# Performance work log

Measured on AMD Instinct MI355X. Metric: run time of the kernel, lower is better.

The kernel has to match this reference:

```python
import jax, jax.numpy as jnp
import numpy as np

B, T, A, H, E = 256, 64, 32, 512, 32


def setup_inputs() -> dict:
    key = jax.random.key(0)
    ks = jax.random.split(key, 8)
    return {
        "actions": jax.random.normal(ks[0], (B, T, A), dtype=jnp.float32),
        "timesteps": jax.random.randint(ks[1], (B,), 0, 1000, dtype=jnp.int32),
        "cat_ids": jax.random.randint(ks[2], (B,), 0, E, dtype=jnp.int32),
        "W1": 0.02 * jax.random.normal(ks[3], (E, A, H), dtype=jnp.float32),
        "b1": jnp.zeros((E, H), dtype=jnp.float32),
        "W2": 0.02 * jax.random.normal(ks[4], (E, 2 * H, H), dtype=jnp.float32),
        "b2": jnp.zeros((E, H), dtype=jnp.float32),
        "W3": 0.02 * jax.random.normal(ks[5], (E, H, H), dtype=jnp.float32),
        "b3": jnp.zeros((E, H), dtype=jnp.float32),
    }


def _cat_linear(x, cat_ids, W, b):
    # per-sample weight gather + bmm, faithful to torch W[cat_ids]; bmm
    return jnp.einsum("btd,bdh->bth", x, W[cat_ids]) + b[cat_ids][:, None, :]


def _sinusoidal(timesteps_bt, dim):
    half = dim // 2
    exponent = -jnp.arange(half, dtype=jnp.float32) * (jnp.log(jnp.float32(10000.0)) / half)
    freqs = timesteps_bt[..., None] * jnp.exp(exponent)  # (B,T,half)
    return jnp.concatenate([jnp.sin(freqs), jnp.cos(freqs)], axis=-1)


def _swish(x):
    return x * jax.nn.sigmoid(x)


def reference(actions, timesteps, cat_ids, W1, b1, W2, b2, W3, b3):
    Bb, Tt, _ = actions.shape
    t_bt = jnp.broadcast_to(timesteps.astype(jnp.float32)[:, None], (Bb, Tt))
    a_emb = _cat_linear(actions, cat_ids, W1, b1)                     # (B,T,H)
    tau_emb = _sinusoidal(t_bt, a_emb.shape[-1]).astype(a_emb.dtype)  # (B,T,H)
    x = jnp.concatenate([a_emb, tau_emb], axis=-1)                    # (B,T,2H)
    x = _swish(_cat_linear(x, cat_ids, W2, b2))
    return _cat_linear(x, cat_ids, W3, b3)
```

## Files before the change

kernel.cpp:

```cpp
#include <hip/hip_runtime.h>
#include <hip/hip_bf16.h>

#define NB 256
#define NT 64
#define NA 32
#define NH 512
#define NE 32
#define MAXTILES 144

typedef short short8 __attribute__((ext_vector_type(8)));
typedef unsigned short ushort8v __attribute__((ext_vector_type(8)));
typedef float f32x4 __attribute__((ext_vector_type(4)));

__device__ __forceinline__ unsigned short f2bf(float f) {
  unsigned int u = __float_as_uint(f);
  u += 0x7FFFu + ((u >> 16) & 1u);
  return (unsigned short)(u >> 16);
}

__device__ __forceinline__ void gl2lds16(const void* g, void* l) {
  __builtin_amdgcn_global_load_lds(
      (const __attribute__((address_space(1))) unsigned int*)g,
      (__attribute__((address_space(3))) unsigned int*)l, 16, 0, 0);
}

__device__ __forceinline__ ushort8v cvt8(float4 a, float4 b) {
  ushort8v t;
  t[0] = f2bf(a.x); t[1] = f2bf(a.y); t[2] = f2bf(a.z); t[3] = f2bf(a.w);
  t[4] = f2bf(b.x); t[5] = f2bf(b.y); t[6] = f2bf(b.z); t[7] = f2bf(b.w);
  return t;
}

__device__ __forceinline__ void pf_w2(float2 (&pf)[8], const float* __restrict__ W2en,
                                      int k0, int tid) {
#pragma unroll
  for (int j = 0; j < 8; j++) {
    int u = j * 256 + tid;
    int kk = u >> 5, cc = u & 31;
    pf[j] = *(const float2*)(W2en + ((size_t)(k0 + kk) << 9) + cc * 2);
  }
}

__device__ __forceinline__ void pf_w1(float4 (&pfw)[2], const float* __restrict__ W1e,
                                      int k0, int tid) {
  int a = tid >> 3, p = tid & 7;
  const float* src = W1e + (size_t)a * NH + k0 + p * 8;
  pfw[0] = *(const float4*)src;
  pfw[1] = *(const float4*)(src + 4);
}

__global__ __launch_bounds__(256) void wp_kernel(
    const float* __restrict__ W1, const float* __restrict__ b1,
    const float* __restrict__ W2, const float* __restrict__ b2,
    const float* __restrict__ W3, const int* __restrict__ timesteps,
    const int* __restrict__ cat, unsigned short* __restrict__ Wt12,
    float* __restrict__ bias2G, float* __restrict__ tvec,
    unsigned short* __restrict__ Wt3, int* __restrict__ tiles,
    int* __restrict__ ntiles_out) {
  __shared__ __align__(16) unsigned char smem[43008];
  int tid = threadIdx.x;
  int bx = blockIdx.x;

  if (bx >= 512 && bx < 2560) {
    float* S = (float*)smem;
    int id = bx - 512;
    int e = id >> 6, rem = id & 63;
    int nt = (rem & 7) * 64, kt = (rem >> 3) * 64;
#pragma unroll
    for (int j = 0; j < 8; j++) {
      int u = j * 256 + tid;
      int k = u >> 5, c = u & 31;
      float2 v = *(const float2*)(W3 + ((size_t)e * 512 + kt + k) * NH + nt + 2 * c);
      *(float2*)(&S[k * 66 + 2 * c]) = v;
    }
    __syncthreads();
#pragma unroll
    for (int j = 0; j < 2; j++) {
      int u = j * 256 + tid;
      int n = u >> 3, c = u & 7;
      ushort8v pk;
#pragma unroll
      for (int jj = 0; jj < 8; jj++) pk[jj] = f2bf(S[(c * 8 + jj) * 66 + n]);
      *(ushort8v*)(Wt3 + ((size_t)e * NH + nt + n) * 512 + kt + c * 8) = pk;
    }
    return;
  }

  if (bx == 2560) {
    int* cnt = (int*)smem;
    int* off = cnt + 32;
    int* cur = off + 32;
    int* order = cur + 32;
    if (tid < NE) cnt[tid] = 0;
    __syncthreads();
    int e = cat[tid];
    atomicAdd(&cnt[e], 1);
    __syncthreads();
    if (tid == 0) {
      int s = 0;
      for (int i = 0; i < NE; i++) { off[i] = s; cur[i] = s; s += cnt[i]; }
    }
    __syncthreads();
    int p = atomicAdd(&cur[e], 1);
    order[p] = tid;
    __syncthreads();
    if (tid == 0) {
      int nt = 0;
      for (int i = 0; i < NE; i++) {
        for (int j = 0; j < cnt[i]; j += 2) {
          tiles[3 * nt + 0] = i;
          tiles[3 * nt + 1] = order[off[i] + j];
          tiles[3 * nt + 2] = (j + 1 < cnt[i]) ? order[off[i] + j + 1] : -1;
          nt++;
        }
      }
      *ntiles_out = nt;
    }
    return;
  }

  int w = tid >> 6, l = tid & 63;
  int lrow = l & 15, kq = l >> 4;
  int tn = tid & 63, tp = tid >> 6;

  if (bx < 256) {
    float* S            = (float*)smem;
    unsigned short* Bs  = (unsigned short*)(smem + 16896);
    unsigned short* As  = (unsigned short*)(smem + 25088);
    float* b1S          = (float*)(smem + 29184);
    float* bias2P       = (float*)(smem + 31232);

    int e = bx >> 3, n0 = (bx & 7) * 64;
    const float* W2en = W2 + ((size_t)e << 19) + n0;
    const float* W1e = W1 + ((size_t)e << 14);

    {
      float2 v = *(const float2*)(b1 + (size_t)e * NH + tid * 2);
      *(float2*)(&b1S[tid * 2]) = v;
    }

    float2 pf[2][8];
    float4 pfW[2][2];
    pf_w2(pf[0], W2en, 0, tid);
    pf_w1(pfW[0], W1e, 0, tid);

    f32x4 acc1[2];
    acc1[0] = (f32x4){0.f, 0.f, 0.f, 0.f};
    acc1[1] = (f32x4){0.f, 0.f, 0.f, 0.f};
    float bacc0 = 0.f, bacc1 = 0.f;

#pragma unroll
    for (int chunk = 0; chunk < 8; chunk++) {
      const int cur = chunk & 1, nxt = cur ^ 1;
      __syncthreads();
#pragma unroll
      for (int j = 0; j < 8; j++) {
        int u = j * 256 + tid;
        int kk = u >> 5, cc = u & 31;
        *(float2*)(&S[kk * 66 + cc * 2]) = pf[cur][j];
      }
      {
        int a = tid >> 3, p = tid & 7;
        *(ushort8v*)(&As[a * 64 + (p ^ (a & 7)) * 8]) = cvt8(pfW[cur][0], pfW[cur][1]);
      }
      if (chunk < 7) {
        pf_w2(pf[nxt], W2en, (chunk + 1) * 64, tid);
        pf_w1(pfW[nxt], W1e, (chunk + 1) * 64, tid);
      }
      __syncthreads();
#pragma unroll
      for (int i2 = 0; i2 < 2; i2++) {
        int p = tp + i2 * 4;
        ushort8v pk;
        float bsum = 0.f;
#pragma unroll
        for (int jj = 0; jj < 8; jj++) {
          float sv = S[(p * 8 + jj) * 66 + tn];
          pk[jj] = f2bf(sv);
          bsum += sv * b1S[chunk * 64 + p * 8 + jj];
        }
        *(ushort8v*)(&Bs[tn * 64 + (p ^ (tn & 7)) * 8]) = pk;
        if (i2 == 0) bacc0 += bsum; else bacc1 += bsum;
      }
      __syncthreads();
#pragma unroll
      for (int s2 = 0; s2 < 2; s2++) {
        int nrow = w * 16 + lrow;
        short8 bf = *(short8*)(&Bs[nrow * 64 + (((s2 * 4 + kq) ^ (nrow & 7))) * 8]);
#pragma unroll
        for (int mi = 0; mi < 2; mi++) {
          int ar = mi * 16 + lrow;
          short8 af = *(short8*)(&As[ar * 64 + (((s2 * 4 + kq) ^ (ar & 7))) * 8]);
          acc1[mi] = __builtin_amdgcn_mfma_f32_16x16x32_bf16(af, bf, acc1[mi], 0, 0, 0);
        }
      }
    }

    unsigned short* Sb = (unsigned short*)S;
#pragma unroll
    for (int mi = 0; mi < 2; mi++)
#pragma unroll
      for (int r = 0; r < 4; r++)
        Sb[(w * 16 + lrow) * 40 + mi * 16 + kq * 4 + r] = f2bf(acc1[mi][r]);
    bias2P[tn * 8 + tp] = bacc0;
    bias2P[tn * 8 + tp + 4] = bacc1;
    __syncthreads();
    if (tid < 64) {
      float s = b2[(size_t)e * NH + n0 + tid];
#pragma unroll
      for (int p2 = 0; p2 < 8; p2++) s += bias2P[tid * 8 + p2];
      bias2G[(size_t)e * NH + n0 + tid] = s;
    }
    {
      int n = tid >> 2, q = tid & 3;
      ushort8v v = *(ushort8v*)(&Sb[n * 40 + q * 8]);
      *(ushort8v*)(Wt12 + ((size_t)(e * NH) + n0 + n) * NA + q * 8) = v;
    }
    return;
  }

  {
    float* S            = (float*)smem;
    unsigned short* Bs  = (unsigned short*)(smem + 16896);
    unsigned short* tauS= (unsigned short*)(smem + 25088);
    int* list           = (int*)(smem + 41728);
    int* pcnt           = (int*)(smem + 42752);

    int id = bx - 256;
    int e = id >> 3, n0 = (id & 7) * 64;
    const float* W2bn = W2 + ((size_t)e << 19) + ((size_t)512 << 9) + n0;

    if (tid == 0) *pcnt = 0;
    __syncthreads();
    {
      int ce = cat[tid];
      if (ce == e) { int p = atomicAdd(pcnt, 1); list[p] = tid; }
    }
    __syncthreads();
    int c = *pcnt;
    if (c == 0) return;

    const float kLog = 0.035977893400931146f;
    float2 pf[2][8];

    for (int sg = 0; sg * 16 < c; sg++) {
      if (sg > 0) __syncthreads();
      for (int j = 0; j < 32; j++) {
        int u = j * 256 + tid;
        int s = u >> 9, k = u & 511;
        int si = sg * 16 + s;
        float t = (si < c) ? (float)timesteps[list[si]] : 0.f;
        float f = expf(-(float)(k & 255) * kLog);
        float ang = t * f;
        tauS[s * 520 + k] = f2bf((k < 256) ? sinf(ang) : cosf(ang));
      }
      pf_w2(pf[0], W2bn, 0, tid);
      f32x4 acc2 = (f32x4){0.f, 0.f, 0.f, 0.f};
#pragma unroll
      for (int chunk = 0; chunk < 8; chunk++) {
        const int cur = chunk & 1, nxt = cur ^ 1;
        __syncthreads();
#pragma unroll
        for (int j = 0; j < 8; j++) {
          int u = j * 256 + tid;
          int kk = u >> 5, cc = u & 31;
          *(float2*)(&S[kk * 66 + cc * 2]) = pf[cur][j];
        }
        if (chunk < 7) pf_w2(pf[nxt], W2bn, (chunk + 1) * 64, tid);
        __syncthreads();
#pragma unroll
        for (int i2 = 0; i2 < 2; i2++) {
          int p = tp + i2 * 4;
          ushort8v pk;
#pragma unroll
          for (int jj = 0; jj < 8; jj++) pk[jj] = f2bf(S[(p * 8 + jj) * 66 + tn]);
          *(ushort8v*)(&Bs[tn * 64 + (p ^ (tn & 7)) * 8]) = pk;
        }
        __syncthreads();
#pragma unroll
        for (int s2 = 0; s2 < 2; s2++) {
          int nrow = w * 16 + lrow;
          short8 bf = *(short8*)(&Bs[nrow * 64 + (((s2 * 4 + kq) ^ (nrow & 7))) * 8]);
          short8 af = *(short8*)(&tauS[lrow * 520 + chunk * 64 + s2 * 32 + kq * 8]);
          acc2 = __builtin_amdgcn_mfma_f32_16x16x32_bf16(af, bf, acc2, 0, 0, 0);
        }
      }
#pragma unroll
      for (int r = 0; r < 4; r++) {
        int si = sg * 16 + kq * 4 + r;
        if (si < c)
          tvec[(size_t)list[si] * NH + n0 + w * 16 + lrow] = acc2[r];
      }
    }
  }
}

__global__ __launch_bounds__(256) void gemmh_kernel(
    const float* __restrict__ actions, const unsigned short* __restrict__ Wt12,
    const float* __restrict__ tvec, const float* __restrict__ bias2,
    const int* __restrict__ cat_ids, unsigned short* __restrict__ Hb) {
  __shared__ __align__(16) unsigned char smem[16384 + 5120 + 33792];
  unsigned short* Ws = (unsigned short*)smem;
  unsigned short* As = (unsigned short*)(smem + 16384);
  unsigned short* Ts = (unsigned short*)(smem + 16384 + 5120);

  int b = blockIdx.y, h = blockIdx.x;
  int tid = threadIdx.x;
  int e = cat_ids[b];

  {
    const unsigned short* wsrc = Wt12 + ((size_t)e * NH + h * 256) * NA;
#pragma unroll
    for (int j = 0; j < 4; j++) {
      int u = j * 256 + tid;
      int n = u >> 2, p = u & 3;
      int ch = p ^ ((n >> 1) & 3);
      gl2lds16(wsrc + (size_t)n * NA + ch * 8,
               Ws + (size_t)(j * 256 + (tid & 448)) * 8);
    }
  }
  {
    int row = tid >> 2, seg = tid & 3;
    const float* src = actions + (size_t)(b * NT + row) * NA + seg * 8;
    float4 v0 = *(const float4*)(src);
    float4 v1 = *(const float4*)(src + 4);
    *(ushort8v*)(&As[row * 40 + seg * 8]) = cvt8(v0, v1);
  }
  __syncthreads();

  int w = tid >> 6, l = tid & 63;
  int lrow = l & 15, kq = l >> 4;
  short8 af = *(short8*)(&As[(w * 16 + lrow) * 40 + kq * 8]);
  f32x4 zero = {0.f, 0.f, 0.f, 0.f};
  f32x4 acc[16];
#pragma unroll
  for (int ni = 0; ni < 16; ni++) {
    int nn = ni * 16 + lrow;
    int p = kq ^ ((nn >> 1) & 3);
    short8 bfv = *(short8*)(&Ws[nn * 32 + p * 8]);
    acc[ni] = __builtin_amdgcn_mfma_f32_16x16x32_bf16(af, bfv, zero, 0, 0, 0);
  }
#pragma unroll
  for (int ni = 0; ni < 16; ni++) {
    int colL = ni * 16 + lrow;
    float bv = tvec[(size_t)b * NH + h * 256 + colL] +
               bias2[(size_t)e * NH + h * 256 + colL];
#pragma unroll
    for (int r = 0; r < 4; r++) {
      int row = w * 16 + kq * 4 + r;
      float v = acc[ni][r] + bv;
      v = v / (1.0f + __expf(-v));
      Ts[row * 264 + colL] = f2bf(v);
    }
  }
  __syncthreads();
#pragma unroll
  for (int i = 0; i < 8; i++) {
    int u = i * 256 + tid;
    int t = u >> 5, c4 = u & 31;
    uint4 v = *(uint4*)(&Ts[t * 264 + c4 * 8]);
    *(uint4*)(Hb + ((size_t)(b * NT + t)) * NH + h * 256 + c4 * 8) = v;
  }
}

template <int KTOT, bool HASTAU, bool SWISH, bool OUT_BF16>
__global__ __launch_bounds__(256) void gemm2_kernel(
    const unsigned short* __restrict__ Xa, const unsigned short* __restrict__ Xt,
    const unsigned short* __restrict__ Wt, const float* __restrict__ bias,
    void* __restrict__ Yv, const int* __restrict__ tiles,
    const int* __restrict__ pntiles) {
  __shared__ __align__(16) unsigned char smem[49152];

  int ti = blockIdx.y;
  if (ti >= *pntiles) return;
  int n0 = blockIdx.x * 64;
  int e = tiles[3 * ti], s0 = tiles[3 * ti + 1], s1 = tiles[3 * ti + 2];
  int s1v = (s1 < 0) ? s0 : s1;

  int tid = threadIdx.x;
  int l = tid & 63;
  int wr = (tid >> 7), wc = (tid >> 6) & 1;
  int lrow = l & 15, kq = l >> 4;

  const unsigned short* wbase = Wt + ((size_t)e * NH + n0) * KTOT;
  constexpr int NIT = KTOT / 64;

  auto stage = [&](int it, int buf) {
    unsigned short* As = (unsigned short*)(smem + buf * 24576);
    unsigned short* Bs = (unsigned short*)(smem + buf * 24576 + 16384);
    int k0 = it * 64;
#pragma unroll
    for (int j = 0; j < 4; j++) {
      int u = j * 256 + tid;
      int row = u >> 3, p = u & 7;
      int ch = p ^ (row & 7);
      int kk = k0 + ch * 8;
      int s = (row < 64) ? s0 : s1v;
      const unsigned short* src;
      if (HASTAU && kk >= 512)
        src = Xt + (size_t)s * NH + (kk - 512);
      else
        src = Xa + ((size_t)(s * NT + (row & 63))) * NH + kk;
      gl2lds16(src, As + (size_t)(j * 256 + (tid & 448)) * 8);
    }
#pragma unroll
    for (int j = 0; j < 2; j++) {
      int u = j * 256 + tid;
      int n = u >> 3, p = u & 7;
      int ch = p ^ (n & 7);
      gl2lds16(wbase + (size_t)n * KTOT + k0 + ch * 8,
               Bs + (size_t)(j * 256 + (tid & 448)) * 8);
    }
  };

  f32x4 acc[4][2];
#pragma unroll
  for (int mi = 0; mi < 4; mi++)
#pragma unroll
    for (int ni = 0; ni < 2; ni++) acc[mi][ni] = (f32x4){0.f, 0.f, 0.f, 0.f};

  stage(0, 0);
  stage(1, 1);

  for (int t = 0; t < NIT; t++) {
    int cur = t & 1;
    unsigned short* As = (unsigned short*)(smem + cur * 24576);
    unsigned short* Bs = (unsigned short*)(smem + cur * 24576 + 16384);

    if (t + 1 < NIT) {
      asm volatile("s_waitcnt vmcnt(6)" ::: "memory");
    } else {
      asm volatile("s_waitcnt vmcnt(0)" ::: "memory");
    }
    __builtin_amdgcn_sched_barrier(0);
    __builtin_amdgcn_s_barrier();
    __builtin_amdgcn_sched_barrier(0);

    short8 afr[2][4], bfr[2][2];
#pragma unroll
    for (int s2 = 0; s2 < 2; s2++) {
#pragma unroll
      for (int mi = 0; mi < 4; mi++) {
        int row = wr * 64 + mi * 16 + lrow;
        int p = (s2 * 4 + kq) ^ (row & 7);
        afr[s2][mi] = *(short8*)(&As[row * 64 + p * 8]);
      }
#pragma unroll
      for (int ni = 0; ni < 2; ni++) {
        int n = wc * 32 + ni * 16 + lrow;
        int p = (s2 * 4 + kq) ^ (n & 7);
        bfr[s2][ni] = *(short8*)(&Bs[n * 64 + p * 8]);
      }
    }
    asm volatile("s_waitcnt lgkmcnt(0)" ::: "memory");
    __builtin_amdgcn_sched_barrier(0);
    __builtin_amdgcn_s_barrier();
    __builtin_amdgcn_sched_barrier(0);

    if (t + 2 < NIT) stage(t + 2, cur);

#pragma unroll
    for (int s2 = 0; s2 < 2; s2++)
#pragma unroll
      for (int mi = 0; mi < 4; mi++)
#pragma unroll
        for (int ni = 0; ni < 2; ni++)
          acc[mi][ni] = __builtin_amdgcn_mfma_f32_16x16x32_bf16(
              afr[s2][mi], bfr[s2][ni], acc[mi][ni], 0, 0, 0);
  }
  __syncthreads();

#pragma unroll
  for (int ni = 0; ni < 2; ni++) {
    int colL = wc * 32 + ni * 16 + lrow;
    float bv = bias[(size_t)e * NH + n0 + colL];
#pragma unroll
    for (int mi = 0; mi < 4; mi++) {
#pragma unroll
      for (int r = 0; r < 4; r++) {
        int row = wr * 64 + mi * 16 + kq * 4 + r;
        float v = acc[mi][ni][r] + bv;
        if (SWISH) v = v / (1.0f + __expf(-v));
        if (OUT_BF16)
          ((unsigned short*)smem)[row * 80 + colL] = f2bf(v);
        else
          ((float*)smem)[row * 68 + colL] = v;
      }
    }
  }
  __syncthreads();
  if (OUT_BF16) {
    unsigned short* Y = (unsigned short*)Yv;
#pragma unroll
    for (int i = 0; i < 4; i++) {
      int u = i * 256 + tid;
      int row = u >> 3, c = u & 7;
      if (row >= 64 && s1 < 0) continue;
      int s = (row < 64) ? s0 : s1;
      uint4 v = *(uint4*)(&((unsigned short*)smem)[row * 80 + c * 8]);
      *(uint4*)(Y + ((size_t)(s * NT + (row & 63))) * NH + n0 + c * 8) = v;
    }
  } else {
    float* Y = (float*)Yv;
#pragma unroll
    for (int i = 0; i < 8; i++) {
      int u = i * 256 + tid;
      int row = u >> 4, c = u & 15;
      if (row >= 64 && s1 < 0) continue;
      int s = (row < 64) ? s0 : s1;
      uint4 v = *(uint4*)(&((float*)smem)[row * 68 + c * 4]);
      *(uint4*)(Y + ((size_t)(s * NT + (row & 63))) * NH + n0 + c * 4) = v;
    }
  }
}

extern "C" void kernel_launch(void* const* d_in, const int* in_sizes, int n_in,
                              void* d_out, int out_size, void* d_ws, size_t ws_size,
                              hipStream_t stream) {
  const float* actions   = (const float*)d_in[0];
  const int*   timesteps = (const int*)d_in[1];
  const int*   cat_ids   = (const int*)d_in[2];
  const float* W1 = (const float*)d_in[3];
  const float* b1 = (const float*)d_in[4];
  const float* W2 = (const float*)d_in[5];
  const float* b2 = (const float*)d_in[6];
  const float* W3 = (const float*)d_in[7];
  const float* b3 = (const float*)d_in[8];

  unsigned short* Hb   = (unsigned short*)d_ws;
  unsigned short* Wt3  = (unsigned short*)((char*)d_ws + (size_t)16777216);
  unsigned short* Wt12 = (unsigned short*)((char*)d_ws + (size_t)33554432);
  float* tvec  = (float*)((char*)d_ws + (size_t)34603008);
  float* bias2 = (float*)((char*)d_ws + (size_t)35127296);
  int* tiles   = (int*)((char*)d_ws + (size_t)35192832);
  int* ntiles  = tiles + 3 * MAXTILES;

  wp_kernel<<<2561, 256, 0, stream>>>(W1, b1, W2, b2, W3, timesteps, cat_ids,
                                      Wt12, bias2, tvec, Wt3, tiles, ntiles);
  gemmh_kernel<<<dim3(2, NB), 256, 0, stream>>>(actions, Wt12, tvec, bias2,
                                                cat_ids, Hb);
  gemm2_kernel<512, false, false, false><<<dim3(8, MAXTILES), 256, 0, stream>>>(
      Hb, nullptr, Wt3, b3, d_out, tiles, ntiles);
}
```

Before: 195.4 us.

## Widen weight-prep blocks to 256 columns and re-tile W3 as k-blocked layout

The weight-prep kernel changes from 64-column tiles over many small blocks to 256-column tiles with a shared streaming helper that pipelines W2 reads two chunks ahead. The W1·W2 fold and tau projection now process 32 rows per pass. The W3 transpose writes a k-blocked [e][kb][n][64] layout, and gemm2 indexes that layout. The goal is fewer blocks, less redundant W1/tau work and more MFMA work per W2 load, at the cost of fewer blocks in flight (641 vs 2561) and more LDS per block.

```diff
diff --git a/kernel.cpp b/kernel.cpp
--- a/kernel.cpp
+++ b/kernel.cpp
@@ -31,25 +31,78 @@
   return t;
 }
 
-__device__ __forceinline__ void pf_w2(float2 (&pf)[8], const float* __restrict__ W2en,
-                                      int k0, int tid) {
+__device__ __forceinline__ void pfld(float2 (&pf)[8], const float* __restrict__ base,
+                                     int c, int tid) {
 #pragma unroll
   for (int j = 0; j < 8; j++) {
     int u = j * 256 + tid;
-    int kk = u >> 5, cc = u & 31;
-    pf[j] = *(const float2*)(W2en + ((size_t)(k0 + kk) << 9) + cc * 2);
-  }
-}
-
-__device__ __forceinline__ void pf_w1(float4 (&pfw)[2], const float* __restrict__ W1e,
-                                      int k0, int tid) {
-  int a = tid >> 3, p = tid & 7;
-  const float* src = W1e + (size_t)a * NH + k0 + p * 8;
-  pfw[0] = *(const float4*)src;
-  pfw[1] = *(const float4*)(src + 4);
-}
-
-__global__ __launch_bounds__(256) void wp_kernel(
+    int kk = u >> 7, cc = u & 127;
+    pf[j] = *(const float2*)(base + (size_t)(c * 16 + kk) * NH + cc * 2);
+  }
+}
+
+template <bool BIASDOT>
+__device__ __forceinline__ void stream_block(
+    const float* __restrict__ Wbase, float* S, unsigned short* Bs,
+    const unsigned short* As, const float* b1S, int tid, int w, int lrow,
+    int kq, f32x4 (&acc)[2][4], float& bacc) {
+  float2 pf[2][8];
+  pfld(pf[0], Wbase, 0, tid);
+  pfld(pf[1], Wbase, 1, tid);
+#pragma unroll 2
+  for (int c = 0; c < 32; c++) {
+    const int cur = c & 1;
+    __syncthreads();
+#pragma unroll
+    for (int j = 0; j < 8; j++) {
+      int u = j * 256 + tid;
+      int kk = u >> 7, cc = u & 127;
+      *(float2*)(&S[kk * 260 + cc * 2]) = pf[cur][j];
+    }
+    if (c + 2 < 32) pfld(pf[cur], Wbase, c + 2, tid);
+    __syncthreads();
+    {
+      int n = tid;
+      ushort8v pk0, pk1;
+#pragma unroll
+      for (int kk = 0; kk < 8; kk++) {
+        float sv = S[kk * 260 + n];
+        pk0[kk] = f2bf(sv);
+        if (BIASDOT) bacc += sv * b1S[c * 16 + kk];
+      }
+#pragma unroll
+      for (int kk = 8; kk < 16; kk++) {
+        float sv = S[kk * 260 + n];
+        pk1[kk - 8] = f2bf(sv);
+        if (BIASDOT) bacc += sv * b1S[c * 16 + kk];
+      }
+      *(ushort8v*)(&Bs[n * 40 + cur * 16]) = pk0;
+      *(ushort8v*)(&Bs[n * 40 + cur * 16 + 8]) = pk1;
+    }
+    if (cur) {
+      __syncthreads();
+      int w2i = c >> 1;
+      short8 bf[4], af[2];
+#pragma unroll
+      for (int ni = 0; ni < 4; ni++)
+        bf[ni] = *(short8*)(&Bs[(w * 64 + ni * 16 + lrow) * 40 + kq * 8]);
+#pragma unroll
+      for (int mi = 0; mi < 2; mi++) {
+        int a = mi * 16 + lrow;
+        int ck = w2i * 4 + kq;
+        af[mi] = *(short8*)(&As[a * 512 + ((ck ^ (a & 7)) << 3)]);
+      }
+#pragma unroll
+      for (int mi = 0; mi < 2; mi++)
+#pragma unroll
+        for (int ni = 0; ni < 4; ni++)
+          acc[mi][ni] = __builtin_amdgcn_mfma_f32_16x16x32_bf16(
+              af[mi], bf[ni], acc[mi][ni], 0, 0, 0);
+    }
+  }
+}
+
+__global__ __launch_bounds__(256) void wp2_kernel(
     const float* __restrict__ W1, const float* __restrict__ b1,
     const float* __restrict__ W2, const float* __restrict__ b2,
     const float* __restrict__ W3, const int* __restrict__ timesteps,
@@ -57,36 +110,52 @@
     float* __restrict__ bias2G, float* __restrict__ tvec,
     unsigned short* __restrict__ Wt3, int* __restrict__ tiles,
     int* __restrict__ ntiles_out) {
-  __shared__ __align__(16) unsigned char smem[43008];
+  __shared__ __align__(16) unsigned char smem[71936];
   int tid = threadIdx.x;
   int bx = blockIdx.x;
 
-  if (bx >= 512 && bx < 2560) {
-    float* S = (float*)smem;
-    int id = bx - 512;
-    int e = id >> 6, rem = id & 63;
-    int nt = (rem & 7) * 64, kt = (rem >> 3) * 64;
-#pragma unroll
-    for (int j = 0; j < 8; j++) {
-      int u = j * 256 + tid;
-      int k = u >> 5, c = u & 31;
-      float2 v = *(const float2*)(W3 + ((size_t)e * 512 + kt + k) * NH + nt + 2 * c);
-      *(float2*)(&S[k * 66 + 2 * c]) = v;
-    }
-    __syncthreads();
-#pragma unroll
-    for (int j = 0; j < 2; j++) {
-      int u = j * 256 + tid;
-      int n = u >> 3, c = u & 7;
-      ushort8v pk;
-#pragma unroll
-      for (int jj = 0; jj < 8; jj++) pk[jj] = f2bf(S[(c * 8 + jj) * 66 + n]);
-      *(ushort8v*)(Wt3 + ((size_t)e * NH + nt + n) * 512 + kt + c * 8) = pk;
+  if (bx >= 128 && bx < 640) {
+    float* S2 = (float*)smem;
+    unsigned short* Bt = (unsigned short*)(smem + 33280);
+    int id = bx - 128;
+    int e = id >> 4, kb = (id >> 1) & 7, nh = id & 1;
+    int kt = kb * 64, nt = nh * 256;
+#pragma unroll
+    for (int h = 0; h < 2; h++) {
+      if (h) __syncthreads();
+#pragma unroll
+      for (int j = 0; j < 16; j++) {
+        int u = j * 256 + tid;
+        int kk = u >> 7, cc = u & 127;
+        float2 v = *(const float2*)(W3 + ((size_t)e * 512 + kt + h * 32 + kk) * NH +
+                                    nt + cc * 2);
+        *(float2*)(&S2[kk * 260 + cc * 2]) = v;
+      }
+      __syncthreads();
+      {
+        int n = tid;
+#pragma unroll
+        for (int q = 0; q < 4; q++) {
+          ushort8v pk;
+#pragma unroll
+          for (int jj = 0; jj < 8; jj++)
+            pk[jj] = f2bf(S2[(q * 8 + jj) * 260 + n]);
+          *(ushort8v*)(&Bt[n * 72 + h * 32 + q * 8]) = pk;
+        }
+      }
+    }
+    __syncthreads();
+    {
+      int n = tid;
+      unsigned short* dst = Wt3 + (((size_t)e * 8 + kb) * 512 + nt + n) * 64;
+#pragma unroll
+      for (int q = 0; q < 8; q++)
+        *(ushort8v*)(dst + q * 8) = *(ushort8v*)(&Bt[n * 72 + q * 8]);
     }
     return;
   }
 
-  if (bx == 2560) {
+  if (bx == 640) {
     int* cnt = (int*)smem;
     int* off = cnt + 32;
     int* cur = off + 32;
@@ -119,178 +188,117 @@
     return;
   }
 
+  float* S           = (float*)smem;
+  unsigned short* Bs = (unsigned short*)(smem + 16640);
+  unsigned short* As = (unsigned short*)(smem + 37120);
+  float* b1S         = (float*)(smem + 69888);
+  int* list          = (int*)(smem + 69888);
+  int* pcnt          = (int*)(smem + 70912);
+
   int w = tid >> 6, l = tid & 63;
   int lrow = l & 15, kq = l >> 4;
-  int tn = tid & 63, tp = tid >> 6;
-
-  if (bx < 256) {
-    float* S            = (float*)smem;
-    unsigned short* Bs  = (unsigned short*)(smem + 16896);
-    unsigned short* As  = (unsigned short*)(smem + 25088);
-    float* b1S          = (float*)(smem + 29184);
-    float* bias2P       = (float*)(smem + 31232);
-
-    int e = bx >> 3, n0 = (bx & 7) * 64;
-    const float* W2en = W2 + ((size_t)e << 19) + n0;
+
+  if (bx < 64) {
+    int e = bx >> 1, nh = bx & 1;
+    const float* Wbase = W2 + ((size_t)e << 19) + nh * 256;
     const float* W1e = W1 + ((size_t)e << 14);
-
     {
       float2 v = *(const float2*)(b1 + (size_t)e * NH + tid * 2);
       *(float2*)(&b1S[tid * 2]) = v;
     }
-
-    float2 pf[2][8];
-    float4 pfW[2][2];
-    pf_w2(pf[0], W2en, 0, tid);
-    pf_w1(pfW[0], W1e, 0, tid);
-
-    f32x4 acc1[2];
-    acc1[0] = (f32x4){0.f, 0.f, 0.f, 0.f};
-    acc1[1] = (f32x4){0.f, 0.f, 0.f, 0.f};
-    float bacc0 = 0.f, bacc1 = 0.f;
-
-#pragma unroll
-    for (int chunk = 0; chunk < 8; chunk++) {
-      const int cur = chunk & 1, nxt = cur ^ 1;
-      __syncthreads();
-#pragma unroll
-      for (int j = 0; j < 8; j++) {
-        int u = j * 256 + tid;
-        int kk = u >> 5, cc = u & 31;
-        *(float2*)(&S[kk * 66 + cc * 2]) = pf[cur][j];
-      }
-      {
-        int a = tid >> 3, p = tid & 7;
-        *(ushort8v*)(&As[a * 64 + (p ^ (a & 7)) * 8]) = cvt8(pfW[cur][0], pfW[cur][1]);
-      }
-      if (chunk < 7) {
-        pf_w2(pf[nxt], W2en, (chunk + 1) * 64, tid);
-        pf_w1(pfW[nxt], W1e, (chunk + 1) * 64, tid);
-      }
-      __syncthreads();
-#pragma unroll
-      for (int i2 = 0; i2 < 2; i2++) {
-        int p = tp + i2 * 4;
-        ushort8v pk;
-        float bsum = 0.f;
-#pragma unroll
-        for (int jj = 0; jj < 8; jj++) {
-          float sv = S[(p * 8 + jj) * 66 + tn];
-          pk[jj] = f2bf(sv);
-          bsum += sv * b1S[chunk * 64 + p * 8 + jj];
-        }
-        *(ushort8v*)(&Bs[tn * 64 + (p ^ (tn & 7)) * 8]) = pk;
-        if (i2 == 0) bacc0 += bsum; else bacc1 += bsum;
-      }
-      __syncthreads();
-#pragma unroll
-      for (int s2 = 0; s2 < 2; s2++) {
-        int nrow = w * 16 + lrow;
-        short8 bf = *(short8*)(&Bs[nrow * 64 + (((s2 * 4 + kq) ^ (nrow & 7))) * 8]);
-#pragma unroll
-        for (int mi = 0; mi < 2; mi++) {
-          int ar = mi * 16 + lrow;
-          short8 af = *(short8*)(&As[ar * 64 + (((s2 * 4 + kq) ^ (ar & 7))) * 8]);
-          acc1[mi] = __builtin_amdgcn_mfma_f32_16x16x32_bf16(af, bf, acc1[mi], 0, 0, 0);
-        }
-      }
-    }
-
-    unsigned short* Sb = (unsigned short*)S;
+    {
+      int a = tid >> 3, seg = tid & 7;
+#pragma unroll
+      for (int p = 0; p < 8; p++) {
+        const float* src = W1e + (size_t)a * NH + p * 64 + seg * 8;
+        float4 v0 = *(const float4*)src;
+        float4 v1 = *(const float4*)(src + 4);
+        int ch = p * 8 + seg;
+        *(ushort8v*)(&As[a * 512 + ((ch ^ (a & 7)) << 3)]) = cvt8(v0, v1);
+      }
+    }
+    f32x4 acc[2][4];
 #pragma unroll
     for (int mi = 0; mi < 2; mi++)
 #pragma unroll
-      for (int r = 0; r < 4; r++)
-        Sb[(w * 16 + lrow) * 40 + mi * 16 + kq * 4 + r] = f2bf(acc1[mi][r]);
-    bias2P[tn * 8 + tp] = bacc0;
-    bias2P[tn * 8 + tp + 4] = bacc1;
-    __syncthreads();
-    if (tid < 64) {
-      float s = b2[(size_t)e * NH + n0 + tid];
-#pragma unroll
-      for (int p2 = 0; p2 < 8; p2++) s += bias2P[tid * 8 + p2];
-      bias2G[(size_t)e * NH + n0 + tid] = s;
-    }
+      for (int ni = 0; ni < 4; ni++) acc[mi][ni] = (f32x4){0.f, 0.f, 0.f, 0.f};
+    float bacc = 0.f;
+    stream_block<true>(Wbase, S, Bs, As, b1S, tid, w, lrow, kq, acc, bacc);
+
+    __syncthreads();
+    unsigned short* Sb = Bs;
+#pragma unroll
+    for (int mi = 0; mi < 2; mi++)
+#pragma unroll
+      for (int ni = 0; ni < 4; ni++)
+#pragma unroll
+        for (int r = 0; r < 4; r++)
+          Sb[(w * 64 + ni * 16 + lrow) * 40 + mi * 16 + kq * 4 + r] =
+              f2bf(acc[mi][ni][r]);
+    bias2G[(size_t)e * NH + nh * 256 + tid] =
+        bacc + b2[(size_t)e * NH + nh * 256 + tid];
+    __syncthreads();
     {
-      int n = tid >> 2, q = tid & 3;
-      ushort8v v = *(ushort8v*)(&Sb[n * 40 + q * 8]);
-      *(ushort8v*)(Wt12 + ((size_t)(e * NH) + n0 + n) * NA + q * 8) = v;
+      int n = tid;
+      unsigned short* dst = Wt12 + ((size_t)e * NH + nh * 256 + n) * NA;
+#pragma unroll
+      for (int q = 0; q < 4; q++)
+        *(ushort8v*)(dst + q * 8) = *(ushort8v*)(&Sb[n * 40 + q * 8]);
     }
     return;
   }
 
   {
-    float* S            = (float*)smem;
-    unsigned short* Bs  = (unsigned short*)(smem + 16896);
-    unsigned short* tauS= (unsigned short*)(smem + 25088);
-    int* list           = (int*)(smem + 41728);
-    int* pcnt           = (int*)(smem + 42752);
-
-    int id = bx - 256;
-    int e = id >> 3, n0 = (id & 7) * 64;
-    const float* W2bn = W2 + ((size_t)e << 19) + ((size_t)512 << 9) + n0;
-
+    int id = bx - 64;
+    int e = id >> 1, nh = id & 1;
+    const float* Wbase = W2 + ((size_t)e << 19) + ((size_t)512 * NH) + nh * 256;
     if (tid == 0) *pcnt = 0;
     __syncthreads();
-    {
-      int ce = cat[tid];
-      if (ce == e) { int p = atomicAdd(pcnt, 1); list[p] = tid; }
-    }
+    if (cat[tid] == e) { int p = atomicAdd(pcnt, 1); list[p] = tid; }
     __syncthreads();
     int c = *pcnt;
     if (c == 0) return;
-
     const float kLog = 0.035977893400931146f;
-    float2 pf[2][8];
-
-    for (int sg = 0; sg * 16 < c; sg++) {
-      if (sg > 0) __syncthreads();
-      for (int j = 0; j < 32; j++) {
-        int u = j * 256 + tid;
-        int s = u >> 9, k = u & 511;
-        int si = sg * 16 + s;
-        float t = (si < c) ? (float)timesteps[list[si]] : 0.f;
-        float f = expf(-(float)(k & 255) * kLog);
-        float ang = t * f;
-        tauS[s * 520 + k] = f2bf((k < 256) ? sinf(ang) : cosf(ang));
-      }
-      pf_w2(pf[0], W2bn, 0, tid);
-      f32x4 acc2 = (f32x4){0.f, 0.f, 0.f, 0.f};
-#pragma unroll
-      for (int chunk = 0; chunk < 8; chunk++) {
-        const int cur = chunk & 1, nxt = cur ^ 1;
-        __syncthreads();
-#pragma unroll
-        for (int j = 0; j < 8; j++) {
-          int u = j * 256 + tid;
-          int kk = u >> 5, cc = u & 31;
-          *(float2*)(&S[kk * 66 + cc * 2]) = pf[cur][j];
+
+    for (int sg = 0; sg * 32 < c; sg++) {
+      if (sg) __syncthreads();
+      {
+        int a = tid >> 3, seg = tid & 7;
+        int si = sg * 32 + a;
+        float tv = (si < c) ? (float)timesteps[list[si]] : 0.f;
+#pragma unroll
+        for (int p = 0; p < 8; p++) {
+          ushort8v pk;
+#pragma unroll
+          for (int q = 0; q < 8; q++) {
+            int k = p * 64 + seg * 8 + q;
+            float f = expf(-(float)(k & 255) * kLog);
+            float ang = tv * f;
+            pk[q] = f2bf((k < 256) ? sinf(ang) : cosf(ang));
+          }
+          int ch = p * 8 + seg;
+          *(ushort8v*)(&As[a * 512 + ((ch ^ (a & 7)) << 3)]) = pk;
         }
-        if (chunk < 7) pf_w2(pf[nxt], W2bn, (chunk + 1) * 64, tid);
-        __syncthreads();
-#pragma unroll
-        for (int i2 = 0; i2 < 2; i2++) {
-          int p = tp + i2 * 4;
-          ushort8v pk;
-#pragma unroll
-          for (int jj = 0; jj < 8; jj++) pk[jj] = f2bf(S[(p * 8 + jj) * 66 + tn]);
-          *(ushort8v*)(&Bs[tn * 64 + (p ^ (tn & 7)) * 8]) = pk;
-        }
-        __syncthreads();
-#pragma unroll
-        for (int s2 = 0; s2 < 2; s2++) {
-          int nrow = w * 16 + lrow;
-          short8 bf = *(short8*)(&Bs[nrow * 64 + (((s2 * 4 + kq) ^ (nrow & 7))) * 8]);
-          short8 af = *(short8*)(&tauS[lrow * 520 + chunk * 64 + s2 * 32 + kq * 8]);
-          acc2 = __builtin_amdgcn_mfma_f32_16x16x32_bf16(af, bf, acc2, 0, 0, 0);
-        }
-      }
-#pragma unroll
-      for (int r = 0; r < 4; r++) {
-        int si = sg * 16 + kq * 4 + r;
-        if (si < c)
-          tvec[(size_t)list[si] * NH + n0 + w * 16 + lrow] = acc2[r];
-      }
+      }
+      f32x4 acc[2][4];
+#pragma unroll
+      for (int mi = 0; mi < 2; mi++)
+#pragma unroll
+        for (int ni = 0; ni < 4; ni++) acc[mi][ni] = (f32x4){0.f, 0.f, 0.f, 0.f};
+      float dummy = 0.f;
+      stream_block<false>(Wbase, S, Bs, As, nullptr, tid, w, lrow, kq, acc, dummy);
+#pragma unroll
+      for (int mi = 0; mi < 2; mi++)
+#pragma unroll
+        for (int ni = 0; ni < 4; ni++)
+#pragma unroll
+          for (int r = 0; r < 4; r++) {
+            int a = mi * 16 + kq * 4 + r;
+            int si = sg * 32 + a;
+            if (si < c)
+              tvec[(size_t)list[si] * NH + nh * 256 + w * 64 + ni * 16 + lrow] =
+                  acc[mi][ni][r];
+          }
     }
   }
 }
@@ -382,7 +390,6 @@
   int wr = (tid >> 7), wc = (tid >> 6) & 1;
   int lrow = l & 15, kq = l >> 4;
 
-  const unsigned short* wbase = Wt + ((size_t)e * NH + n0) * KTOT;
   constexpr int NIT = KTOT / 64;
 
   auto stage = [&](int it, int buf) {
@@ -408,7 +415,7 @@
       int u = j * 256 + tid;
       int n = u >> 3, p = u & 7;
       int ch = p ^ (n & 7);
-      gl2lds16(wbase + (size_t)n * KTOT + k0 + ch * 8,
+      gl2lds16(Wt + (((size_t)e * 8 + it) * 512 + n0 + n) * 64 + ch * 8,
                Bs + (size_t)(j * 256 + (tid & 448)) * 8);
     }
   };
@@ -535,7 +542,7 @@
   int* tiles   = (int*)((char*)d_ws + (size_t)35192832);
   int* ntiles  = tiles + 3 * MAXTILES;
 
-  wp_kernel<<<2561, 256, 0, stream>>>(W1, b1, W2, b2, W3, timesteps, cat_ids,
+  wp2_kernel<<<641, 256, 0, stream>>>(W1, b1, W2, b2, W3, timesteps, cat_ids,
                                       Wt12, bias2, tvec, Wt3, tiles, ntiles);
   gemmh_kernel<<<dim3(2, NB), 256, 0, stream>>>(actions, Wt12, tvec, bias2,
                                                 cat_ids, Hb);
```

Result: no change. 193.5 us (-1.0%).
